# Performance work log

Hardware: AMD Instinct MI355X
Metric: run time of the kernel (lower is better)

## Reference

```python
import jax, jax.numpy as jnp
import numpy as np
from jax.scipy.linalg import expm

N_MODES, N_LAYERS, CUTOFF, BATCH = 6, 6, 3, 1024
M2 = N_MODES * (N_MODES - 1) // 2                  # beamsplitter thetas per interferometer
N_IF = N_MODES * (N_MODES - 1) + (N_MODES - 1)     # interferometer param count = 35

_np_a = np.diag(np.sqrt(np.arange(1, CUTOFF)), 1)  # truncated annihilation operator
A = jnp.asarray(_np_a, jnp.complex64)
AD = A.conj().T
NVEC = jnp.arange(CUTOFF, dtype=jnp.float32)       # number operator diagonal
X_OP = A + AD                                      # x quadrature (hbar=2, PennyLane/SF convention)
BS_GEN = jnp.kron(AD, A) - jnp.kron(A, AD)         # Beamsplitter(theta, 0) generator
SQ_GEN = A @ A - AD @ AD                           # Squeezing(r, 0) generator (times r/2)
D_GEN = AD - A                                     # Displacement(r, 0) generator

def disp_gate(r):
    return expm(r.astype(jnp.complex64) * D_GEN)

def sq_gate(r):
    return expm(0.5 * r.astype(jnp.complex64) * SQ_GEN)

def bs_gate(theta):
    return expm(theta.astype(jnp.complex64) * BS_GEN)

def apply_1(psi, U, m):
    # psi: (B, D, ..., D); apply DxD gate U on mode m
    psi = jnp.moveaxis(psi, 1 + m, -1)
    psi = psi @ U.T
    return jnp.moveaxis(psi, -1, 1 + m)

def apply_1_batched(psi, U, m):
    # U: (B, D, D) per-sample gate (data-encoding displacement)
    psi = jnp.moveaxis(psi, 1 + m, -1)
    psi = jnp.einsum('b...j,bij->b...i', psi, U)
    return jnp.moveaxis(psi, -1, 1 + m)

def apply_2(psi, U, m):
    psi = jnp.moveaxis(psi, (1 + m, 2 + m), (-2, -1))
    sh = psi.shape
    psi = (psi.reshape(sh[:-2] + (CUTOFF * CUTOFF,)) @ U.T).reshape(sh)
    return jnp.moveaxis(psi, (-2, -1), (1 + m, 2 + m))

def apply_diag(psi, d, m):
    shape = [1] * psi.ndim
    shape[1 + m] = CUTOFF
    return psi * d.reshape(shape)

def interferometer(psi, params):
    theta = params[:M2]
    rphi = params[-N_MODES:]  # faithful to source: overlaps last (unused) phi param
    n = 0
    for l in range(N_MODES):
        for k in range(N_MODES - 1):
            if (l + k) % 2 != 1:
                psi = apply_2(psi, bs_gate(theta[n]), k)
                n += 1
    for i in range(max(1, N_MODES - 1)):
        psi = apply_diag(psi, jnp.exp(1j * rphi[i] * NVEC), i)
    return psi

def cv_forward(x, theta_1, theta_2, squeezing_r, displacement_r, kerr_params):
    B = x.shape[0]
    psi = jnp.zeros((B,) + (CUTOFF,) * N_MODES, jnp.complex64)
    psi = psi.at[(slice(None),) + (0,) * N_MODES].set(1.0)  # |0...0> vacuum
    for m in range(N_MODES):  # data-encoding displacements, per-sample gates
        psi = apply_1_batched(psi, jax.vmap(disp_gate)(x[:, m]), m)
    for L in range(N_LAYERS):
        psi = interferometer(psi, theta_1[L])
        for m in range(N_MODES):
            psi = apply_1(psi, sq_gate(squeezing_r[L, m] * 0.5), m)
        psi = interferometer(psi, theta_2[L])
        for m in range(N_MODES):
            psi = apply_1(psi, disp_gate(displacement_r[L, m]), m)
            psi = apply_diag(psi, jnp.exp(1j * (kerr_params[L, m] * 0.001) * NVEC * NVEC), m)
    sum_axes = tuple(range(1, psi.ndim))
    outs = [jnp.sum(jnp.conj(psi) * apply_1(psi, X_OP, m), axis=sum_axes).real
            for m in range(N_MODES)]
    return jnp.stack(outs, axis=1)  # (B, N_MODES)

def setup_inputs() -> dict:
    key = jax.random.key(0)
    ks = jax.random.split(key, 6)
    passive_sd = 0.01 * np.pi
    return {
        'x': jax.random.normal(ks[0], (BATCH, N_MODES), jnp.float32),
        'theta_1': jax.random.normal(ks[1], (N_LAYERS, N_IF), jnp.float32) * passive_sd,
        'theta_2': jax.random.normal(ks[2], (N_LAYERS, N_IF), jnp.float32) * np.float32(0.2 * np.pi),
        'squeezing_r': jax.random.normal(ks[3], (N_LAYERS, N_MODES), jnp.float32) * 1e-3,
        'displacement_r': jax.random.normal(ks[4], (N_LAYERS, N_MODES), jnp.float32) * 1e-3,
        'kerr_params': jax.random.normal(ks[5], (N_LAYERS, N_MODES), jnp.float32) * 1e-3,
    }

def reference(x, theta_1, theta_2, squeezing_r, displacement_r, kerr_params):
    return cv_forward(x, theta_1, theta_2, squeezing_r, displacement_r, kerr_params)
```

## Files before the change

kernel.cpp:

```cpp
#include <hip/hip_runtime.h>

#define SQRT2f 1.41421356237309515f
#define SQRT3f 1.73205080756887729f

__device__ __forceinline__ float2 cmul(float2 a, float2 b) {
  return make_float2(a.x*b.x - a.y*b.y, a.x*b.y + a.y*b.x);
}
__device__ __forceinline__ float2 cadd(float2 a, float2 b) {
  return make_float2(a.x + b.x, a.y + b.y);
}

__device__ __forceinline__ void bs_q(float2 q[9], float2 cs) {
  const float c = cs.x, s = cs.y;
  const float c2 = c*c - s*s, s2 = 2.f*c*s;
  const float cc = c*c, ss = s*s, rcs = SQRT2f*c*s;
  float2 a1=q[1], a3=q[3], a2=q[2], a4=q[4], a6=q[6], a5=q[5], a7=q[7];
  q[1] = make_float2(c*a1.x - s*a3.x, c*a1.y - s*a3.y);
  q[3] = make_float2(s*a1.x + c*a3.x, s*a1.y + c*a3.y);
  q[2] = make_float2(cc*a2.x - rcs*a4.x + ss*a6.x, cc*a2.y - rcs*a4.y + ss*a6.y);
  q[4] = make_float2(rcs*a2.x + c2*a4.x - rcs*a6.x, rcs*a2.y + c2*a4.y - rcs*a6.y);
  q[6] = make_float2(ss*a2.x + rcs*a4.x + cc*a6.x, ss*a2.y + rcs*a4.y + cc*a6.y);
  q[5] = make_float2(c2*a5.x - s2*a7.x, c2*a5.y - s2*a7.y);
  q[7] = make_float2(s2*a5.x + c2*a7.x, s2*a5.y + c2*a7.y);
}

template<int SP>
__device__ __forceinline__ void bs_nonet(float2* __restrict__ psi, int base,
                                         float2 cs) {
  const float c = cs.x, s = cs.y;
  const float c2 = c*c - s*s, s2 = 2.f*c*s;
  const float cc = c*c, ss = s*s, rcs = SQRT2f*c*s;
  float2 a1 = psi[base+SP],   a3 = psi[base+3*SP];
  float2 a2 = psi[base+2*SP], a4 = psi[base+4*SP], a6 = psi[base+6*SP];
  float2 a5 = psi[base+5*SP], a7 = psi[base+7*SP];
  psi[base+SP]   = make_float2(c*a1.x - s*a3.x, c*a1.y - s*a3.y);
  psi[base+3*SP] = make_float2(s*a1.x + c*a3.x, s*a1.y + c*a3.y);
  psi[base+2*SP] = make_float2(cc*a2.x - rcs*a4.x + ss*a6.x,
                               cc*a2.y - rcs*a4.y + ss*a6.y);
  psi[base+4*SP] = make_float2(rcs*a2.x + c2*a4.x - rcs*a6.x,
                               rcs*a2.y + c2*a4.y - rcs*a6.y);
  psi[base+6*SP] = make_float2(ss*a2.x + rcs*a4.x + cc*a6.x,
                               ss*a2.y + rcs*a4.y + cc*a6.y);
  psi[base+5*SP] = make_float2(c2*a5.x - s2*a7.x, c2*a5.y - s2*a7.y);
  psi[base+7*SP] = make_float2(s2*a5.x + c2*a7.x, s2*a5.y + c2*a7.y);
}

template<int SP>
__device__ __forceinline__ void dpbs_nonet(float2* __restrict__ psi, int base,
                                           const float2* __restrict__ G,
                                           float2 cs) {
  const float2* A = G; const float2* B = G + 9;
  float2 v[3][3];
#pragma unroll
  for (int j = 0; j < 3; ++j)
#pragma unroll
    for (int jb = 0; jb < 3; ++jb) v[j][jb] = psi[base + j*3*SP + jb*SP];
  float2 t[3][3];
#pragma unroll
  for (int j = 0; j < 3; ++j)
#pragma unroll
    for (int ib = 0; ib < 3; ++ib)
      t[j][ib] = cadd(cadd(cmul(B[ib*3+0],v[j][0]), cmul(B[ib*3+1],v[j][1])),
                      cmul(B[ib*3+2],v[j][2]));
  float2 q[9];
#pragma unroll
  for (int i = 0; i < 3; ++i)
#pragma unroll
    for (int ib = 0; ib < 3; ++ib)
      q[i*3+ib] = cadd(cadd(cmul(A[i*3+0],t[0][ib]), cmul(A[i*3+1],t[1][ib])),
                       cmul(A[i*3+2],t[2][ib]));
  bs_q(q, cs);
#pragma unroll
  for (int i = 0; i < 3; ++i)
#pragma unroll
    for (int ib = 0; ib < 3; ++ib) psi[base + i*3*SP + ib*SP] = q[i*3+ib];
}

template<int SP>
__device__ __forceinline__ void sqbs_nonet(float2* __restrict__ psi, int base,
                                           const float2* __restrict__ G,
                                           float2 cs) {
  float2 A00=G[0],A02=G[1],A11=G[2],A20=G[3],A22=G[4];
  float2 B00=G[5],B02=G[6],B11=G[7],B20=G[8],B22=G[9];
  float2 v[3][3];
#pragma unroll
  for (int j = 0; j < 3; ++j)
#pragma unroll
    for (int jb = 0; jb < 3; ++jb) v[j][jb] = psi[base + j*3*SP + jb*SP];
  float2 t[3][3];
#pragma unroll
  for (int j = 0; j < 3; ++j) {
    t[j][0] = cadd(cmul(B00,v[j][0]), cmul(B02,v[j][2]));
    t[j][1] = cmul(B11,v[j][1]);
    t[j][2] = cadd(cmul(B20,v[j][0]), cmul(B22,v[j][2]));
  }
  float2 q[9];
#pragma unroll
  for (int ib = 0; ib < 3; ++ib) {
    q[ib]   = cadd(cmul(A00,t[0][ib]), cmul(A02,t[2][ib]));
    q[3+ib] = cmul(A11,t[1][ib]);
    q[6+ib] = cadd(cmul(A20,t[0][ib]), cmul(A22,t[2][ib]));
  }
  bs_q(q, cs);
#pragma unroll
  for (int i = 0; i < 3; ++i)
#pragma unroll
    for (int ib = 0; ib < 3; ++ib) psi[base + i*3*SP + ib*SP] = q[i*3+ib];
}

#define BASE4(g, s0,s1,s2,s3) ({ int _d=(g); int _b=(_d%3)*(s0); _d/=3; \
  _b += (_d%3)*(s1); _d/=3; _b += (_d%3)*(s2); _d/=3; _b += (_d%3)*(s3); _b; })
#define BASE5(g, s0,s1,s2,s3,s4) ({ int _d=(g); int _b=(_d%3)*(s0); _d/=3; \
  _b += (_d%3)*(s1); _d/=3; _b += (_d%3)*(s2); _d/=3; _b += (_d%3)*(s3); _d/=3; \
  _b += (_d%3)*(s4); _b; })

__device__ __forceinline__ float2 dpk_entry(const float* __restrict__ dr,
                                            const float* __restrict__ th2,
                                            const float* __restrict__ kp,
                                            int L, int mode, int i, int j) {
  float sn, cn; sincosf(SQRT3f*dr[L*6+mode], &sn, &cn);
  float sw = sn*(1.f/SQRT3f), cw = (1.f-cn)*(1.f/3.f);
  float U;
  if      (i==0) U = (j==0) ? (1.f-cw)     : (j==1) ? (-sw)         : (SQRT2f*cw);
  else if (i==1) U = (j==0) ? (sw)         : (j==1) ? (1.f-3.f*cw)  : (-SQRT2f*sw);
  else           U = (j==0) ? (SQRT2f*cw)  : (j==1) ? (SQRT2f*sw)   : (1.f-2.f*cw);
  float2 ph = make_float2(1.f, 0.f);
  if (mode < 5) { float ps, pc; sincosf(th2[L*35+29+mode], &ps, &pc);
                  ph = make_float2(pc, ps); }
  float2 phj = (j==0) ? make_float2(1.f,0.f) : (j==1) ? ph : cmul(ph, ph);
  float ks, kc; sincosf(0.001f*kp[L*6+mode], &ks, &kc);
  float2 k1 = make_float2(kc, ks);
  float2 ki = (i==0) ? make_float2(1.f,0.f)
            : (i==1) ? k1 : cmul(cmul(k1,k1), cmul(k1,k1));
  float2 t = cmul(phj, ki);
  return make_float2(U*t.x, U*t.y);
}

__global__ __launch_bounds__(128)
void cvnn_kernel(const float* __restrict__ x,
                 const float* __restrict__ th1,
                 const float* __restrict__ th2,
                 const float* __restrict__ sr,
                 const float* __restrict__ dr,
                 const float* __restrict__ kp,
                 float* __restrict__ out) {
  __shared__ float2 psi[729];
  __shared__ float2 gtab[690];
  __shared__ float red[12];

  const int tid = threadIdx.x;
  const int bidx = blockIdx.x;

  for (int f = tid; f < 690; f += 128) {
    float sn, cn; float2 v;
    if (f < 180) {
      int Lp = f/15, pos = f%15;
      int L = Lp/2, pass = Lp%2;
      float th = (pass ? th2 : th1)[L*35 + pos];
      sincosf(th, &sn, &cn); v = make_float2(cn, sn);
    } else if (f < 360) {
      int i = f - 180; int Lc = i/10, e = i%10;
      int L = Lc/3, c3 = Lc%3;
      int mode = 2*c3 + (e >= 5); int ee = e%5;
      float Sq, Cq; sincosf(0.25f*SQRT2f*sr[L*6+mode], &Sq, &Cq);
      float2 ph = make_float2(1.f, 0.f);
      if (mode < 5) { float ps, pc; sincosf(th1[L*35+29+mode], &ps, &pc);
                      ph = make_float2(pc, ps); }
      float2 ph2 = cmul(ph, ph);
      if      (ee == 0) v = make_float2(Cq, 0.f);
      else if (ee == 1) v = make_float2(Sq*ph2.x, Sq*ph2.y);
      else if (ee == 2) v = ph;
      else if (ee == 3) v = make_float2(-Sq, 0.f);
      else              v = make_float2(Cq*ph2.x, Cq*ph2.y);
    } else if (f < 630) {
      int i = f - 360; int Ld = i/18, e = i%18;
      int Ls = Ld/3, c3 = Ld%3;
      int mode = 2*c3 + (e >= 9); int ee = e%9;
      v = dpk_entry(dr, th2, kp, Ls, mode, ee/3, ee%3);
    } else if (f < 684) {
      int i = f - 630; int m = i/9, e = i%9;
      int ii = e/3, jj = e%3;
      float2 D0i = dpk_entry(dr, th2, kp, 5, m, 0, ii);
      float2 D1i = dpk_entry(dr, th2, kp, 5, m, 1, ii);
      float2 D2i = dpk_entry(dr, th2, kp, 5, m, 2, ii);
      float2 D0j = dpk_entry(dr, th2, kp, 5, m, 0, jj);
      float2 D1j = dpk_entry(dr, th2, kp, 5, m, 1, jj);
      float2 D2j = dpk_entry(dr, th2, kp, 5, m, 2, jj);
      float2 c0 = make_float2(D0i.x, -D0i.y);
      float2 c1 = make_float2(D1i.x, -D1i.y);
      float2 c2 = make_float2(D2i.x, -D2i.y);
      float2 acc = cmul(c0, D1j);
      float2 tmp = make_float2(D0j.x + SQRT2f*D2j.x, D0j.y + SQRT2f*D2j.y);
      acc = cadd(acc, cmul(c1, tmp));
      acc = cadd(acc, cmul(c2, make_float2(SQRT2f*D1j.x, SQRT2f*D1j.y)));
      v = acc;
    } else {
      int mode = f - 684;
      sincosf(SQRT3f*x[bidx*6 + mode], &sn, &cn);
      v = make_float2(sn*(1.f/SQRT3f), (1.f-cn)*(1.f/3.f));
    }
    gtab[f] = v;
  }
  __syncthreads();

  for (int idx = tid; idx < 729; idx += 128) {
    float pr = 1.f; int d = idx;
#pragma unroll
    for (int mm = 5; mm >= 0; --mm) {
      int n = d % 3; d /= 3;
      float2 dc = gtab[684 + mm];
      pr *= (n==0) ? (1.f-dc.y) : (n==1) ? dc.x : SQRT2f*dc.y;
    }
    psi[idx] = make_float2(pr, 0.f);
  }

  const bool act = (tid < 81);
  const int g = (tid < 81) ? tid : 0;
  const int b0 = g;
  const int b1 = BASE4(g, 1, 3, 9, 243);
  const int b2 = BASE4(g, 1, 3, 81, 243);
  const int b3 = BASE4(g, 1, 27, 81, 243);
  const int b4 = BASE4(g, 9, 27, 81, 243);
  __syncthreads();

  float2 csN = gtab[0];
  __syncthreads();

#define BSP(SP, BB, NEXT)  { if (act) bs_nonet<SP>(psi, BB, csN); \
    csN = gtab[NEXT]; __syncthreads(); }
#define DPBS(SP, BB, GI, NEXT) { if (act) dpbs_nonet<SP>(psi, BB, &gtab[GI], csN); \
    csN = gtab[NEXT]; __syncthreads(); }
#define SQBS(SP, BB, GI, NEXT) { if (act) sqbs_nonet<SP>(psi, BB, &gtab[GI], csN); \
    csN = gtab[NEXT]; __syncthreads(); }

#pragma unroll
  for (int L = 0; L < 6; ++L) {
    const int i1 = (L*2)*15, i2 = (L*2+1)*15;
    if (L == 0) {
      BSP(81, b0, i1+1); BSP(9, b2, i1+2); BSP(1, b4, i1+3);
    } else {
      const int gd = 360 + (L-1)*3*18;
      DPBS(81, b0, gd+0,  i1+1); DPBS(9, b2, gd+18, i1+2); DPBS(1, b4, gd+36, i1+3);
    }
    BSP(27, b1, i1+4);  BSP(3, b3, i1+5);
    BSP(81, b0, i1+6);  BSP(9, b2, i1+7);  BSP(1, b4, i1+8);
    BSP(27, b1, i1+9);  BSP(3, b3, i1+10);
    BSP(81, b0, i1+11); BSP(9, b2, i1+12); BSP(1, b4, i1+13);
    BSP(27, b1, i1+14); BSP(3, b3, i2+0);
    {
      const int gs = 180 + L*3*10;
      SQBS(81, b0, gs+0, i2+1); SQBS(9, b2, gs+10, i2+2); SQBS(1, b4, gs+20, i2+3);
    }
    BSP(27, b1, i2+4);  BSP(3, b3, i2+5);
    BSP(81, b0, i2+6);  BSP(9, b2, i2+7);  BSP(1, b4, i2+8);
    BSP(27, b1, i2+9);  BSP(3, b3, i2+10);
    BSP(81, b0, i2+11); BSP(9, b2, i2+12); BSP(1, b4, i2+13);
    BSP(27, b1, i2+14); BSP(3, b3, (L < 5) ? (L+1)*30 : 0);
  }

  float xs[6] = {0.f, 0.f, 0.f, 0.f, 0.f, 0.f};
  for (int it = 0; it < 2; ++it) {
    int t = tid + (it << 7);
    if (t < 243) {
#define XACC(m, SS, BB) { int b_ = (BB); \
      float2 a_ = psi[b_]; float2 e_ = psi[b_+(SS)]; float2 f_ = psi[b_+2*(SS)]; \
      const float2* M_ = &gtab[630 + (m)*9]; \
      float d0 = M_[0].x, d1 = M_[4].x, d2 = M_[8].x; \
      float2 M01 = M_[1], M02 = M_[2], M12 = M_[5]; \
      xs[m] += d0*(a_.x*a_.x + a_.y*a_.y) + d1*(e_.x*e_.x + e_.y*e_.y) \
             + d2*(f_.x*f_.x + f_.y*f_.y) \
        + 2.f*(M01.x*(a_.x*e_.x + a_.y*e_.y) - M01.y*(a_.x*e_.y - a_.y*e_.x)) \
        + 2.f*(M02.x*(a_.x*f_.x + a_.y*f_.y) - M02.y*(a_.x*f_.y - a_.y*f_.x)) \
        + 2.f*(M12.x*(e_.x*f_.x + e_.y*f_.y) - M12.y*(e_.x*f_.y - e_.y*f_.x)); }
      XACC(0, 243, BASE5(t, 1, 3, 9, 27, 81));
      XACC(1, 81,  BASE5(t, 1, 3, 9, 27, 243));
      XACC(2, 27,  BASE5(t, 1, 3, 9, 81, 243));
      XACC(3, 9,   BASE5(t, 1, 3, 27, 81, 243));
      XACC(4, 3,   BASE5(t, 1, 9, 27, 81, 243));
      XACC(5, 1,   BASE5(t, 3, 9, 27, 81, 243));
    }
  }
  const int lane = tid & 63, wid = tid >> 6;
#pragma unroll
  for (int m = 0; m < 6; ++m) {
    float v = xs[m];
    for (int off = 32; off > 0; off >>= 1) v += __shfl_down(v, off);
    if (lane == 0) red[wid*6 + m] = v;
  }
  __syncthreads();
  if (tid < 6) out[bidx*6 + tid] = red[tid] + red[6 + tid];
}

extern "C" void kernel_launch(void* const* d_in, const int* in_sizes, int n_in,
                              void* d_out, int out_size, void* d_ws, size_t ws_size,
                              hipStream_t stream) {
  const float* x  = (const float*)d_in[0];
  const float* t1 = (const float*)d_in[1];
  const float* t2 = (const float*)d_in[2];
  const float* sr = (const float*)d_in[3];
  const float* dr = (const float*)d_in[4];
  const float* kp = (const float*)d_in[5];
  const int B = in_sizes[0] / 6;
  cvnn_kernel<<<B, 128, 0, stream>>>(x, t1, t2, sr, dr, kp, (float*)d_out);
}
```

Before: 92.86 us.

## Process two batch samples per block to amortize gate table setup and barriers

Each block now simulates two batch samples, with separate shared-memory state vectors, instead of one. The gate table built from the shared parameters is computed once per pair, and each barrier-separated gate step updates both states using the same coefficients. This halves the grid size and the per-sample cost of table construction and synchronisation. The trade-off is doubled per-thread register and shared-memory use, which may lower occupancy, and only half as many blocks to fill the device.

```diff
diff --git a/kernel.cpp b/kernel.cpp
--- a/kernel.cpp
+++ b/kernel.cpp
@@ -10,10 +10,9 @@
   return make_float2(a.x + b.x, a.y + b.y);
 }
 
-__device__ __forceinline__ void bs_q(float2 q[9], float2 cs) {
-  const float c = cs.x, s = cs.y;
-  const float c2 = c*c - s*s, s2 = 2.f*c*s;
-  const float cc = c*c, ss = s*s, rcs = SQRT2f*c*s;
+__device__ __forceinline__ void bs_q(float2 q[9], float c, float s,
+                                     float c2, float s2, float cc, float ss,
+                                     float rcs) {
   float2 a1=q[1], a3=q[3], a2=q[2], a4=q[4], a6=q[6], a5=q[5], a7=q[7];
   q[1] = make_float2(c*a1.x - s*a3.x, c*a1.y - s*a3.y);
   q[3] = make_float2(s*a1.x + c*a3.x, s*a1.y + c*a3.y);
@@ -25,87 +24,155 @@
 }
 
 template<int SP>
-__device__ __forceinline__ void bs_nonet(float2* __restrict__ psi, int base,
-                                         float2 cs) {
+__device__ __forceinline__ void bs_nonet2(float2* __restrict__ pA,
+                                          float2* __restrict__ pB,
+                                          int base, float2 cs) {
   const float c = cs.x, s = cs.y;
   const float c2 = c*c - s*s, s2 = 2.f*c*s;
   const float cc = c*c, ss = s*s, rcs = SQRT2f*c*s;
-  float2 a1 = psi[base+SP],   a3 = psi[base+3*SP];
-  float2 a2 = psi[base+2*SP], a4 = psi[base+4*SP], a6 = psi[base+6*SP];
-  float2 a5 = psi[base+5*SP], a7 = psi[base+7*SP];
-  psi[base+SP]   = make_float2(c*a1.x - s*a3.x, c*a1.y - s*a3.y);
-  psi[base+3*SP] = make_float2(s*a1.x + c*a3.x, s*a1.y + c*a3.y);
-  psi[base+2*SP] = make_float2(cc*a2.x - rcs*a4.x + ss*a6.x,
-                               cc*a2.y - rcs*a4.y + ss*a6.y);
-  psi[base+4*SP] = make_float2(rcs*a2.x + c2*a4.x - rcs*a6.x,
-                               rcs*a2.y + c2*a4.y - rcs*a6.y);
-  psi[base+6*SP] = make_float2(ss*a2.x + rcs*a4.x + cc*a6.x,
-                               ss*a2.y + rcs*a4.y + cc*a6.y);
-  psi[base+5*SP] = make_float2(c2*a5.x - s2*a7.x, c2*a5.y - s2*a7.y);
-  psi[base+7*SP] = make_float2(s2*a5.x + c2*a7.x, s2*a5.y + c2*a7.y);
+  float2 A1 = pA[base+SP],   A3 = pA[base+3*SP];
+  float2 A2 = pA[base+2*SP], A4 = pA[base+4*SP], A6 = pA[base+6*SP];
+  float2 A5 = pA[base+5*SP], A7 = pA[base+7*SP];
+  float2 B1 = pB[base+SP],   B3 = pB[base+3*SP];
+  float2 B2 = pB[base+2*SP], B4 = pB[base+4*SP], B6 = pB[base+6*SP];
+  float2 B5 = pB[base+5*SP], B7 = pB[base+7*SP];
+  pA[base+SP]   = make_float2(c*A1.x - s*A3.x, c*A1.y - s*A3.y);
+  pA[base+3*SP] = make_float2(s*A1.x + c*A3.x, s*A1.y + c*A3.y);
+  pA[base+2*SP] = make_float2(cc*A2.x - rcs*A4.x + ss*A6.x,
+                              cc*A2.y - rcs*A4.y + ss*A6.y);
+  pA[base+4*SP] = make_float2(rcs*A2.x + c2*A4.x - rcs*A6.x,
+                              rcs*A2.y + c2*A4.y - rcs*A6.y);
+  pA[base+6*SP] = make_float2(ss*A2.x + rcs*A4.x + cc*A6.x,
+                              ss*A2.y + rcs*A4.y + cc*A6.y);
+  pA[base+5*SP] = make_float2(c2*A5.x - s2*A7.x, c2*A5.y - s2*A7.y);
+  pA[base+7*SP] = make_float2(s2*A5.x + c2*A7.x, s2*A5.y + c2*A7.y);
+  pB[base+SP]   = make_float2(c*B1.x - s*B3.x, c*B1.y - s*B3.y);
+  pB[base+3*SP] = make_float2(s*B1.x + c*B3.x, s*B1.y + c*B3.y);
+  pB[base+2*SP] = make_float2(cc*B2.x - rcs*B4.x + ss*B6.x,
+                              cc*B2.y - rcs*B4.y + ss*B6.y);
+  pB[base+4*SP] = make_float2(rcs*B2.x + c2*B4.x - rcs*B6.x,
+                              rcs*B2.y + c2*B4.y - rcs*B6.y);
+  pB[base+6*SP] = make_float2(ss*B2.x + rcs*B4.x + cc*B6.x,
+                              ss*B2.y + rcs*B4.y + cc*B6.y);
+  pB[base+5*SP] = make_float2(c2*B5.x - s2*B7.x, c2*B5.y - s2*B7.y);
+  pB[base+7*SP] = make_float2(s2*B5.x + c2*B7.x, s2*B5.y + c2*B7.y);
 }
 
 template<int SP>
-__device__ __forceinline__ void dpbs_nonet(float2* __restrict__ psi, int base,
-                                           const float2* __restrict__ G,
-                                           float2 cs) {
+__device__ __forceinline__ void dpbs_nonet2(float2* __restrict__ pA,
+                                            float2* __restrict__ pB,
+                                            int base,
+                                            const float2* __restrict__ G,
+                                            float2 cs) {
+  const float c = cs.x, s = cs.y;
+  const float c2 = c*c - s*s, s2 = 2.f*c*s;
+  const float cc = c*c, ss = s*s, rcs = SQRT2f*c*s;
   const float2* A = G; const float2* B = G + 9;
-  float2 v[3][3];
+  float2 vA[3][3], vB[3][3];
 #pragma unroll
   for (int j = 0; j < 3; ++j)
 #pragma unroll
-    for (int jb = 0; jb < 3; ++jb) v[j][jb] = psi[base + j*3*SP + jb*SP];
-  float2 t[3][3];
-#pragma unroll
-  for (int j = 0; j < 3; ++j)
-#pragma unroll
-    for (int ib = 0; ib < 3; ++ib)
-      t[j][ib] = cadd(cadd(cmul(B[ib*3+0],v[j][0]), cmul(B[ib*3+1],v[j][1])),
-                      cmul(B[ib*3+2],v[j][2]));
-  float2 q[9];
-#pragma unroll
-  for (int i = 0; i < 3; ++i)
-#pragma unroll
-    for (int ib = 0; ib < 3; ++ib)
-      q[i*3+ib] = cadd(cadd(cmul(A[i*3+0],t[0][ib]), cmul(A[i*3+1],t[1][ib])),
-                       cmul(A[i*3+2],t[2][ib]));
-  bs_q(q, cs);
-#pragma unroll
-  for (int i = 0; i < 3; ++i)
-#pragma unroll
-    for (int ib = 0; ib < 3; ++ib) psi[base + i*3*SP + ib*SP] = q[i*3+ib];
+    for (int jb = 0; jb < 3; ++jb) {
+      vA[j][jb] = pA[base + j*3*SP + jb*SP];
+      vB[j][jb] = pB[base + j*3*SP + jb*SP];
+    }
+  float2 qA[9], qB[9];
+  {
+    float2 t[3][3];
+#pragma unroll
+    for (int j = 0; j < 3; ++j)
+#pragma unroll
+      for (int ib = 0; ib < 3; ++ib)
+        t[j][ib] = cadd(cadd(cmul(B[ib*3+0],vA[j][0]), cmul(B[ib*3+1],vA[j][1])),
+                        cmul(B[ib*3+2],vA[j][2]));
+#pragma unroll
+    for (int i = 0; i < 3; ++i)
+#pragma unroll
+      for (int ib = 0; ib < 3; ++ib)
+        qA[i*3+ib] = cadd(cadd(cmul(A[i*3+0],t[0][ib]), cmul(A[i*3+1],t[1][ib])),
+                          cmul(A[i*3+2],t[2][ib]));
+  }
+  {
+    float2 t[3][3];
+#pragma unroll
+    for (int j = 0; j < 3; ++j)
+#pragma unroll
+      for (int ib = 0; ib < 3; ++ib)
+        t[j][ib] = cadd(cadd(cmul(B[ib*3+0],vB[j][0]), cmul(B[ib*3+1],vB[j][1])),
+                        cmul(B[ib*3+2],vB[j][2]));
+#pragma unroll
+    for (int i = 0; i < 3; ++i)
+#pragma unroll
+      for (int ib = 0; ib < 3; ++ib)
+        qB[i*3+ib] = cadd(cadd(cmul(A[i*3+0],t[0][ib]), cmul(A[i*3+1],t[1][ib])),
+                          cmul(A[i*3+2],t[2][ib]));
+  }
+  bs_q(qA, c, s, c2, s2, cc, ss, rcs);
+  bs_q(qB, c, s, c2, s2, cc, ss, rcs);
+#pragma unroll
+  for (int i = 0; i < 9; ++i) {
+    pA[base + (i/3)*3*SP + (i%3)*SP] = qA[i];
+    pB[base + (i/3)*3*SP + (i%3)*SP] = qB[i];
+  }
 }
 
 template<int SP>
-__device__ __forceinline__ void sqbs_nonet(float2* __restrict__ psi, int base,
-                                           const float2* __restrict__ G,
-                                           float2 cs) {
+__device__ __forceinline__ void sqbs_nonet2(float2* __restrict__ pA,
+                                            float2* __restrict__ pB,
+                                            int base,
+                                            const float2* __restrict__ G,
+                                            float2 cs) {
+  const float c = cs.x, s = cs.y;
+  const float c2 = c*c - s*s, s2 = 2.f*c*s;
+  const float cc = c*c, ss = s*s, rcs = SQRT2f*c*s;
   float2 A00=G[0],A02=G[1],A11=G[2],A20=G[3],A22=G[4];
   float2 B00=G[5],B02=G[6],B11=G[7],B20=G[8],B22=G[9];
-  float2 v[3][3];
+  float2 vA[3][3], vB[3][3];
 #pragma unroll
   for (int j = 0; j < 3; ++j)
 #pragma unroll
-    for (int jb = 0; jb < 3; ++jb) v[j][jb] = psi[base + j*3*SP + jb*SP];
-  float2 t[3][3];
-#pragma unroll
-  for (int j = 0; j < 3; ++j) {
-    t[j][0] = cadd(cmul(B00,v[j][0]), cmul(B02,v[j][2]));
-    t[j][1] = cmul(B11,v[j][1]);
-    t[j][2] = cadd(cmul(B20,v[j][0]), cmul(B22,v[j][2]));
-  }
-  float2 q[9];
-#pragma unroll
-  for (int ib = 0; ib < 3; ++ib) {
-    q[ib]   = cadd(cmul(A00,t[0][ib]), cmul(A02,t[2][ib]));
-    q[3+ib] = cmul(A11,t[1][ib]);
-    q[6+ib] = cadd(cmul(A20,t[0][ib]), cmul(A22,t[2][ib]));
-  }
-  bs_q(q, cs);
-#pragma unroll
-  for (int i = 0; i < 3; ++i)
-#pragma unroll
-    for (int ib = 0; ib < 3; ++ib) psi[base + i*3*SP + ib*SP] = q[i*3+ib];
+    for (int jb = 0; jb < 3; ++jb) {
+      vA[j][jb] = pA[base + j*3*SP + jb*SP];
+      vB[j][jb] = pB[base + j*3*SP + jb*SP];
+    }
+  float2 qA[9], qB[9];
+  {
+    float2 t[3][3];
+#pragma unroll
+    for (int j = 0; j < 3; ++j) {
+      t[j][0] = cadd(cmul(B00,vA[j][0]), cmul(B02,vA[j][2]));
+      t[j][1] = cmul(B11,vA[j][1]);
+      t[j][2] = cadd(cmul(B20,vA[j][0]), cmul(B22,vA[j][2]));
+    }
+#pragma unroll
+    for (int ib = 0; ib < 3; ++ib) {
+      qA[ib]   = cadd(cmul(A00,t[0][ib]), cmul(A02,t[2][ib]));
+      qA[3+ib] = cmul(A11,t[1][ib]);
+      qA[6+ib] = cadd(cmul(A20,t[0][ib]), cmul(A22,t[2][ib]));
+    }
+  }
+  {
+    float2 t[3][3];
+#pragma unroll
+    for (int j = 0; j < 3; ++j) {
+      t[j][0] = cadd(cmul(B00,vB[j][0]), cmul(B02,vB[j][2]));
+      t[j][1] = cmul(B11,vB[j][1]);
+      t[j][2] = cadd(cmul(B20,vB[j][0]), cmul(B22,vB[j][2]));
+    }
+#pragma unroll
+    for (int ib = 0; ib < 3; ++ib) {
+      qB[ib]   = cadd(cmul(A00,t[0][ib]), cmul(A02,t[2][ib]));
+      qB[3+ib] = cmul(A11,t[1][ib]);
+      qB[6+ib] = cadd(cmul(A20,t[0][ib]), cmul(A22,t[2][ib]));
+    }
+  }
+  bs_q(qA, c, s, c2, s2, cc, ss, rcs);
+  bs_q(qB, c, s, c2, s2, cc, ss, rcs);
+#pragma unroll
+  for (int i = 0; i < 9; ++i) {
+    pA[base + (i/3)*3*SP + (i%3)*SP] = qA[i];
+    pB[base + (i/3)*3*SP + (i%3)*SP] = qB[i];
+  }
 }
 
 #define BASE4(g, s0,s1,s2,s3) ({ int _d=(g); int _b=(_d%3)*(s0); _d/=3; \
@@ -143,15 +210,16 @@
                  const float* __restrict__ sr,
                  const float* __restrict__ dr,
                  const float* __restrict__ kp,
-                 float* __restrict__ out) {
-  __shared__ float2 psi[729];
-  __shared__ float2 gtab[690];
-  __shared__ float red[12];
+                 float* __restrict__ out, int Btot) {
+  __shared__ float2 psiA[729];
+  __shared__ float2 psiB[729];
+  __shared__ float2 gtab[696];
+  __shared__ float red[24];
 
   const int tid = threadIdx.x;
   const int bidx = blockIdx.x;
 
-  for (int f = tid; f < 690; f += 128) {
+  for (int f = tid; f < 696; f += 128) {
     float sn, cn; float2 v;
     if (f < 180) {
       int Lp = f/15, pos = f%15;
@@ -195,8 +263,9 @@
       acc = cadd(acc, cmul(c2, make_float2(SQRT2f*D1j.x, SQRT2f*D1j.y)));
       v = acc;
     } else {
-      int mode = f - 684;
-      sincosf(SQRT3f*x[bidx*6 + mode], &sn, &cn);
+      int i = f - 684; int st = i/6, mode = i%6;
+      int b = bidx*2 + st; if (b >= Btot) b = Btot - 1;
+      sincosf(SQRT3f*x[b*6 + mode], &sn, &cn);
       v = make_float2(sn*(1.f/SQRT3f), (1.f-cn)*(1.f/3.f));
     }
     gtab[f] = v;
@@ -204,14 +273,17 @@
   __syncthreads();
 
   for (int idx = tid; idx < 729; idx += 128) {
-    float pr = 1.f; int d = idx;
+    float prA = 1.f, prB = 1.f; int d = idx;
 #pragma unroll
     for (int mm = 5; mm >= 0; --mm) {
       int n = d % 3; d /= 3;
-      float2 dc = gtab[684 + mm];
-      pr *= (n==0) ? (1.f-dc.y) : (n==1) ? dc.x : SQRT2f*dc.y;
-    }
-    psi[idx] = make_float2(pr, 0.f);
+      float2 dA = gtab[684 + mm];
+      float2 dB = gtab[690 + mm];
+      prA *= (n==0) ? (1.f-dA.y) : (n==1) ? dA.x : SQRT2f*dA.y;
+      prB *= (n==0) ? (1.f-dB.y) : (n==1) ? dB.x : SQRT2f*dB.y;
+    }
+    psiA[idx] = make_float2(prA, 0.f);
+    psiB[idx] = make_float2(prB, 0.f);
   }
 
   const bool act = (tid < 81);
@@ -226,11 +298,11 @@
   float2 csN = gtab[0];
   __syncthreads();
 
-#define BSP(SP, BB, NEXT)  { if (act) bs_nonet<SP>(psi, BB, csN); \
+#define BSP(SP, BB, NEXT)  { if (act) bs_nonet2<SP>(psiA, psiB, BB, csN); \
     csN = gtab[NEXT]; __syncthreads(); }
-#define DPBS(SP, BB, GI, NEXT) { if (act) dpbs_nonet<SP>(psi, BB, &gtab[GI], csN); \
+#define DPBS(SP, BB, GI, NEXT) { if (act) dpbs_nonet2<SP>(psiA, psiB, BB, &gtab[GI], csN); \
     csN = gtab[NEXT]; __syncthreads(); }
-#define SQBS(SP, BB, GI, NEXT) { if (act) sqbs_nonet<SP>(psi, BB, &gtab[GI], csN); \
+#define SQBS(SP, BB, GI, NEXT) { if (act) sqbs_nonet2<SP>(psiA, psiB, BB, &gtab[GI], csN); \
     csN = gtab[NEXT]; __syncthreads(); }
 
 #pragma unroll
@@ -258,37 +330,51 @@
     BSP(27, b1, i2+14); BSP(3, b3, (L < 5) ? (L+1)*30 : 0);
   }
 
-  float xs[6] = {0.f, 0.f, 0.f, 0.f, 0.f, 0.f};
+  float xsA[6] = {0.f,0.f,0.f,0.f,0.f,0.f};
+  float xsB[6] = {0.f,0.f,0.f,0.f,0.f,0.f};
   for (int it = 0; it < 2; ++it) {
     int t = tid + (it << 7);
     if (t < 243) {
-#define XACC(m, SS, BB) { int b_ = (BB); \
-      float2 a_ = psi[b_]; float2 e_ = psi[b_+(SS)]; float2 f_ = psi[b_+2*(SS)]; \
+#define XACC2(m, SS, BB) { int b_ = (BB); \
       const float2* M_ = &gtab[630 + (m)*9]; \
       float d0 = M_[0].x, d1 = M_[4].x, d2 = M_[8].x; \
       float2 M01 = M_[1], M02 = M_[2], M12 = M_[5]; \
-      xs[m] += d0*(a_.x*a_.x + a_.y*a_.y) + d1*(e_.x*e_.x + e_.y*e_.y) \
-             + d2*(f_.x*f_.x + f_.y*f_.y) \
-        + 2.f*(M01.x*(a_.x*e_.x + a_.y*e_.y) - M01.y*(a_.x*e_.y - a_.y*e_.x)) \
-        + 2.f*(M02.x*(a_.x*f_.x + a_.y*f_.y) - M02.y*(a_.x*f_.y - a_.y*f_.x)) \
-        + 2.f*(M12.x*(e_.x*f_.x + e_.y*f_.y) - M12.y*(e_.x*f_.y - e_.y*f_.x)); }
-      XACC(0, 243, BASE5(t, 1, 3, 9, 27, 81));
-      XACC(1, 81,  BASE5(t, 1, 3, 9, 27, 243));
-      XACC(2, 27,  BASE5(t, 1, 3, 9, 81, 243));
-      XACC(3, 9,   BASE5(t, 1, 3, 27, 81, 243));
-      XACC(4, 3,   BASE5(t, 1, 9, 27, 81, 243));
-      XACC(5, 1,   BASE5(t, 3, 9, 27, 81, 243));
+      { float2 a_ = psiA[b_]; float2 e_ = psiA[b_+(SS)]; float2 f_ = psiA[b_+2*(SS)]; \
+        xsA[m] += d0*(a_.x*a_.x + a_.y*a_.y) + d1*(e_.x*e_.x + e_.y*e_.y) \
+               + d2*(f_.x*f_.x + f_.y*f_.y) \
+          + 2.f*(M01.x*(a_.x*e_.x + a_.y*e_.y) - M01.y*(a_.x*e_.y - a_.y*e_.x)) \
+          + 2.f*(M02.x*(a_.x*f_.x + a_.y*f_.y) - M02.y*(a_.x*f_.y - a_.y*f_.x)) \
+          + 2.f*(M12.x*(e_.x*f_.x + e_.y*f_.y) - M12.y*(e_.x*f_.y - e_.y*f_.x)); } \
+      { float2 a_ = psiB[b_]; float2 e_ = psiB[b_+(SS)]; float2 f_ = psiB[b_+2*(SS)]; \
+        xsB[m] += d0*(a_.x*a_.x + a_.y*a_.y) + d1*(e_.x*e_.x + e_.y*e_.y) \
+               + d2*(f_.x*f_.x + f_.y*f_.y) \
+          + 2.f*(M01.x*(a_.x*e_.x + a_.y*e_.y) - M01.y*(a_.x*e_.y - a_.y*e_.x)) \
+          + 2.f*(M02.x*(a_.x*f_.x + a_.y*f_.y) - M02.y*(a_.x*f_.y - a_.y*f_.x)) \
+          + 2.f*(M12.x*(e_.x*f_.x + e_.y*f_.y) - M12.y*(e_.x*f_.y - e_.y*f_.x)); } }
+      XACC2(0, 243, BASE5(t, 1, 3, 9, 27, 81));
+      XACC2(1, 81,  BASE5(t, 1, 3, 9, 27, 243));
+      XACC2(2, 27,  BASE5(t, 1, 3, 9, 81, 243));
+      XACC2(3, 9,   BASE5(t, 1, 3, 27, 81, 243));
+      XACC2(4, 3,   BASE5(t, 1, 9, 27, 81, 243));
+      XACC2(5, 1,   BASE5(t, 3, 9, 27, 81, 243));
     }
   }
   const int lane = tid & 63, wid = tid >> 6;
 #pragma unroll
   for (int m = 0; m < 6; ++m) {
-    float v = xs[m];
-    for (int off = 32; off > 0; off >>= 1) v += __shfl_down(v, off);
-    if (lane == 0) red[wid*6 + m] = v;
+    float vA = xsA[m], vB = xsB[m];
+    for (int off = 32; off > 0; off >>= 1) {
+      vA += __shfl_down(vA, off); vB += __shfl_down(vB, off);
+    }
+    if (lane == 0) { red[wid*6 + m] = vA; red[12 + wid*6 + m] = vB; }
   }
   __syncthreads();
-  if (tid < 6) out[bidx*6 + tid] = red[tid] + red[6 + tid];
+  if (tid < 12) {
+    int st = tid/6, m = tid%6;
+    float v = red[st*12 + m] + red[st*12 + 6 + m];
+    int b = bidx*2 + st;
+    if (b < Btot) out[b*6 + m] = v;
+  }
 }
 
 extern "C" void kernel_launch(void* const* d_in, const int* in_sizes, int n_in,
@@ -301,5 +387,6 @@
   const float* dr = (const float*)d_in[4];
   const float* kp = (const float*)d_in[5];
   const int B = in_sizes[0] / 6;
-  cvnn_kernel<<<B, 128, 0, stream>>>(x, t1, t2, sr, dr, kp, (float*)d_out);
-}
+  const int nb = (B + 1) / 2;
+  cvnn_kernel<<<nb, 128, 0, stream>>>(x, t1, t2, sr, dr, kp, (float*)d_out, B);
+}
```

Measured after the change: 128.8 us. 38.7% more time.

## Fuse beamsplitter stages into 27-element cube sweeps to cut barrier count

Applied to the files above, without the earlier changes.

Replaces the per-beamsplitter passes (one 81-thread pass and one barrier per gate) with grouped passes. Each of 27 threads loads a 27-element sub-cube over three modes and applies two or three consecutive gates in registers, including the folded displacement/squeezing matrices. The number of shared-memory round trips and __syncthreads per layer falls from 15 to 9. In exchange, only 27 threads are active in those phases, so parallelism drops and register pressure rises because each thread holds 27 complex values.

```diff
diff --git a/kernel.cpp b/kernel.cpp
--- a/kernel.cpp
+++ b/kernel.cpp
@@ -10,10 +10,9 @@
   return make_float2(a.x + b.x, a.y + b.y);
 }
 
-__device__ __forceinline__ void bs_q(float2 q[9], float2 cs) {
-  const float c = cs.x, s = cs.y;
-  const float c2 = c*c - s*s, s2 = 2.f*c*s;
-  const float cc = c*c, ss = s*s, rcs = SQRT2f*c*s;
+__device__ __forceinline__ void bs_q(float2* q, float c, float s,
+                                     float c2, float s2, float cc, float ss,
+                                     float rcs) {
   float2 a1=q[1], a3=q[3], a2=q[2], a4=q[4], a6=q[6], a5=q[5], a7=q[7];
   q[1] = make_float2(c*a1.x - s*a3.x, c*a1.y - s*a3.y);
   q[3] = make_float2(s*a1.x + c*a3.x, s*a1.y + c*a3.y);
@@ -46,70 +45,144 @@
 }
 
 template<int SP>
+__device__ __forceinline__ void sqbs_nonet(float2* __restrict__ psi, int base,
+                                           const float2* __restrict__ G,
+                                           float2 cs) {
+  const float c = cs.x, s = cs.y;
+  const float c2 = c*c - s*s, s2 = 2.f*c*s;
+  const float cc = c*c, ss = s*s, rcs = SQRT2f*c*s;
+  float2 A00=G[0],A02=G[1],A11=G[2],A20=G[3],A22=G[4];
+  float2 B00=G[5],B02=G[6],B11=G[7],B20=G[8],B22=G[9];
+  float2 v[3][3];
+#pragma unroll
+  for (int j = 0; j < 3; ++j)
+#pragma unroll
+    for (int jb = 0; jb < 3; ++jb) v[j][jb] = psi[base + j*3*SP + jb*SP];
+  float2 q[9];
+  {
+    float2 t[3][3];
+#pragma unroll
+    for (int j = 0; j < 3; ++j) {
+      t[j][0] = cadd(cmul(B00,v[j][0]), cmul(B02,v[j][2]));
+      t[j][1] = cmul(B11,v[j][1]);
+      t[j][2] = cadd(cmul(B20,v[j][0]), cmul(B22,v[j][2]));
+    }
+#pragma unroll
+    for (int ib = 0; ib < 3; ++ib) {
+      q[ib]   = cadd(cmul(A00,t[0][ib]), cmul(A02,t[2][ib]));
+      q[3+ib] = cmul(A11,t[1][ib]);
+      q[6+ib] = cadd(cmul(A20,t[0][ib]), cmul(A22,t[2][ib]));
+    }
+  }
+  bs_q(q, c, s, c2, s2, cc, ss, rcs);
+#pragma unroll
+  for (int i = 0; i < 9; ++i) psi[base + (i/3)*3*SP + (i%3)*SP] = q[i];
+}
+
+template<int SP>
 __device__ __forceinline__ void dpbs_nonet(float2* __restrict__ psi, int base,
                                            const float2* __restrict__ G,
                                            float2 cs) {
+  const float c = cs.x, s = cs.y;
+  const float c2 = c*c - s*s, s2 = 2.f*c*s;
+  const float cc = c*c, ss = s*s, rcs = SQRT2f*c*s;
   const float2* A = G; const float2* B = G + 9;
   float2 v[3][3];
 #pragma unroll
   for (int j = 0; j < 3; ++j)
 #pragma unroll
     for (int jb = 0; jb < 3; ++jb) v[j][jb] = psi[base + j*3*SP + jb*SP];
-  float2 t[3][3];
-#pragma unroll
-  for (int j = 0; j < 3; ++j)
-#pragma unroll
-    for (int ib = 0; ib < 3; ++ib)
-      t[j][ib] = cadd(cadd(cmul(B[ib*3+0],v[j][0]), cmul(B[ib*3+1],v[j][1])),
-                      cmul(B[ib*3+2],v[j][2]));
   float2 q[9];
-#pragma unroll
-  for (int i = 0; i < 3; ++i)
-#pragma unroll
-    for (int ib = 0; ib < 3; ++ib)
-      q[i*3+ib] = cadd(cadd(cmul(A[i*3+0],t[0][ib]), cmul(A[i*3+1],t[1][ib])),
-                       cmul(A[i*3+2],t[2][ib]));
-  bs_q(q, cs);
-#pragma unroll
-  for (int i = 0; i < 3; ++i)
-#pragma unroll
-    for (int ib = 0; ib < 3; ++ib) psi[base + i*3*SP + ib*SP] = q[i*3+ib];
-}
-
-template<int SP>
-__device__ __forceinline__ void sqbs_nonet(float2* __restrict__ psi, int base,
+  {
+    float2 t[3][3];
+#pragma unroll
+    for (int j = 0; j < 3; ++j)
+#pragma unroll
+      for (int ib = 0; ib < 3; ++ib)
+        t[j][ib] = cadd(cadd(cmul(B[ib*3+0],v[j][0]), cmul(B[ib*3+1],v[j][1])),
+                        cmul(B[ib*3+2],v[j][2]));
+#pragma unroll
+    for (int i = 0; i < 3; ++i)
+#pragma unroll
+      for (int ib = 0; ib < 3; ++ib)
+        q[i*3+ib] = cadd(cadd(cmul(A[i*3+0],t[0][ib]), cmul(A[i*3+1],t[1][ib])),
+                         cmul(A[i*3+2],t[2][ib]));
+  }
+  bs_q(q, c, s, c2, s2, cc, ss, rcs);
+#pragma unroll
+  for (int i = 0; i < 9; ++i) psi[base + (i/3)*3*SP + (i%3)*SP] = q[i];
+}
+
+template<int ST, int FOLD>
+__device__ __forceinline__ void cube_sweep(float2* __restrict__ psi, int base,
                                            const float2* __restrict__ G,
-                                           float2 cs) {
-  float2 A00=G[0],A02=G[1],A11=G[2],A20=G[3],A22=G[4];
-  float2 B00=G[5],B02=G[6],B11=G[7],B20=G[8],B22=G[9];
-  float2 v[3][3];
-#pragma unroll
-  for (int j = 0; j < 3; ++j)
-#pragma unroll
-    for (int jb = 0; jb < 3; ++jb) v[j][jb] = psi[base + j*3*SP + jb*SP];
-  float2 t[3][3];
-#pragma unroll
-  for (int j = 0; j < 3; ++j) {
-    t[j][0] = cadd(cmul(B00,v[j][0]), cmul(B02,v[j][2]));
-    t[j][1] = cmul(B11,v[j][1]);
-    t[j][2] = cadd(cmul(B20,v[j][0]), cmul(B22,v[j][2]));
-  }
-  float2 q[9];
-#pragma unroll
-  for (int ib = 0; ib < 3; ++ib) {
-    q[ib]   = cadd(cmul(A00,t[0][ib]), cmul(A02,t[2][ib]));
-    q[3+ib] = cmul(A11,t[1][ib]);
-    q[6+ib] = cadd(cmul(A20,t[0][ib]), cmul(A22,t[2][ib]));
-  }
-  bs_q(q, cs);
-#pragma unroll
-  for (int i = 0; i < 3; ++i)
-#pragma unroll
-    for (int ib = 0; ib < 3; ++ib) psi[base + i*3*SP + ib*SP] = q[i*3+ib];
-}
-
-#define BASE4(g, s0,s1,s2,s3) ({ int _d=(g); int _b=(_d%3)*(s0); _d/=3; \
-  _b += (_d%3)*(s1); _d/=3; _b += (_d%3)*(s2); _d/=3; _b += (_d%3)*(s3); _b; })
+                                           float2 csM, float2 csH) {
+  float2 v[27];
+#pragma unroll
+  for (int r = 0; r < 27; ++r) v[r] = psi[base + ST*r];
+  if (FOLD == 1) {
+    float2 A00=G[0],A02=G[1],A11=G[2],A20=G[3],A22=G[4];
+    float2 B00=G[5],B02=G[6],B11=G[7],B20=G[8],B22=G[9];
+#pragma unroll
+    for (int t = 0; t < 9; ++t) {
+      float2 u0=v[t*3], u2=v[t*3+2];
+      v[t*3]   = cadd(cmul(B00,u0), cmul(B02,u2));
+      v[t*3+1] = cmul(B11, v[t*3+1]);
+      v[t*3+2] = cadd(cmul(B20,u0), cmul(B22,u2));
+    }
+#pragma unroll
+    for (int h = 0; h < 3; ++h)
+#pragma unroll
+      for (int lo = 0; lo < 3; ++lo) {
+        int rb = h*9 + lo;
+        float2 u0=v[rb], u2=v[rb+6];
+        v[rb]   = cadd(cmul(A00,u0), cmul(A02,u2));
+        v[rb+3] = cmul(A11, v[rb+3]);
+        v[rb+6] = cadd(cmul(A20,u0), cmul(A22,u2));
+      }
+  }
+  if (FOLD == 2) {
+#pragma unroll
+    for (int t = 0; t < 9; ++t) {
+      float2 u0=v[t*3], u1=v[t*3+1], u2=v[t*3+2];
+      v[t*3]   = cadd(cadd(cmul(G[9+0],u0),cmul(G[9+1],u1)),cmul(G[9+2],u2));
+      v[t*3+1] = cadd(cadd(cmul(G[9+3],u0),cmul(G[9+4],u1)),cmul(G[9+5],u2));
+      v[t*3+2] = cadd(cadd(cmul(G[9+6],u0),cmul(G[9+7],u1)),cmul(G[9+8],u2));
+    }
+#pragma unroll
+    for (int h = 0; h < 3; ++h)
+#pragma unroll
+      for (int lo = 0; lo < 3; ++lo) {
+        int rb = h*9 + lo;
+        float2 u0=v[rb], u1=v[rb+3], u2=v[rb+6];
+        v[rb]   = cadd(cadd(cmul(G[0],u0),cmul(G[1],u1)),cmul(G[2],u2));
+        v[rb+3] = cadd(cadd(cmul(G[3],u0),cmul(G[4],u1)),cmul(G[5],u2));
+        v[rb+6] = cadd(cadd(cmul(G[6],u0),cmul(G[7],u1)),cmul(G[8],u2));
+      }
+  }
+  {
+    const float c=csM.x, s=csM.y;
+    const float c2=c*c-s*s, s2=2.f*c*s, cc=c*c, ss=s*s, rcs=SQRT2f*c*s;
+#pragma unroll
+    for (int h = 0; h < 3; ++h) bs_q(&v[h*9], c, s, c2, s2, cc, ss, rcs);
+  }
+  {
+    const float c=csH.x, s=csH.y;
+    const float c2=c*c-s*s, s2=2.f*c*s, cc=c*c, ss=s*s, rcs=SQRT2f*c*s;
+#pragma unroll
+    for (int lo = 0; lo < 3; ++lo) {
+      float2 q[9];
+#pragma unroll
+      for (int j = 0; j < 9; ++j) q[j] = v[(j/3)*9 + (j%3)*3 + lo];
+      bs_q(q, c, s, c2, s2, cc, ss, rcs);
+#pragma unroll
+      for (int j = 0; j < 9; ++j) v[(j/3)*9 + (j%3)*3 + lo] = q[j];
+    }
+  }
+#pragma unroll
+  for (int r = 0; r < 27; ++r) psi[base + ST*r] = v[r];
+}
+
 #define BASE5(g, s0,s1,s2,s3,s4) ({ int _d=(g); int _b=(_d%3)*(s0); _d/=3; \
   _b += (_d%3)*(s1); _d/=3; _b += (_d%3)*(s2); _d/=3; _b += (_d%3)*(s3); _d/=3; \
   _b += (_d%3)*(s4); _b; })
@@ -214,59 +287,69 @@
     psi[idx] = make_float2(pr, 0.f);
   }
 
-  const bool act = (tid < 81);
   const int g = (tid < 81) ? tid : 0;
   const int b0 = g;
-  const int b1 = BASE4(g, 1, 3, 9, 243);
-  const int b2 = BASE4(g, 1, 3, 81, 243);
-  const int b3 = BASE4(g, 1, 27, 81, 243);
-  const int b4 = BASE4(g, 9, 27, 81, 243);
+  const int h = (tid < 27) ? tid : 0;
+  const int n0h = h/9, hm = (h%9)/3, hl = h%3;
+  const int base123 = n0h*243 + hm*3 + hl;
+  const int base345 = n0h*243 + hm*81 + hl*27;
   __syncthreads();
 
-  float2 csN = gtab[0];
-  __syncthreads();
-
-#define BSP(SP, BB, NEXT)  { if (act) bs_nonet<SP>(psi, BB, csN); \
-    csN = gtab[NEXT]; __syncthreads(); }
-#define DPBS(SP, BB, GI, NEXT) { if (act) dpbs_nonet<SP>(psi, BB, &gtab[GI], csN); \
-    csN = gtab[NEXT]; __syncthreads(); }
-#define SQBS(SP, BB, GI, NEXT) { if (act) sqbs_nonet<SP>(psi, BB, &gtab[GI], csN); \
-    csN = gtab[NEXT]; __syncthreads(); }
+#define W81_BS(GI)      { if (tid < 81) bs_nonet<81>(psi, b0, gtab[GI]); \
+    __syncthreads(); }
+#define W81_SQBS(GS,GI) { if (tid < 81) sqbs_nonet<81>(psi, b0, &gtab[GS], gtab[GI]); \
+    __syncthreads(); }
+#define W81_DPBS(GD,GI) { if (tid < 81) dpbs_nonet<81>(psi, b0, &gtab[GD], gtab[GI]); \
+    __syncthreads(); }
+#define W27_123(F,GP,GI1,GI2) { if (tid < 27) \
+    cube_sweep<9,F>(psi, base123, GP, gtab[GI1], gtab[GI2]); __syncthreads(); }
+#define W27_345(F,GP,GI1,GI2) { if (tid < 27) \
+    cube_sweep<1,F>(psi, base345, GP, gtab[GI1], gtab[GI2]); __syncthreads(); }
 
 #pragma unroll
   for (int L = 0; L < 6; ++L) {
-    const int i1 = (L*2)*15, i2 = (L*2+1)*15;
-    if (L == 0) {
-      BSP(81, b0, i1+1); BSP(9, b2, i1+2); BSP(1, b4, i1+3);
-    } else {
-      const int gd = 360 + (L-1)*3*18;
-      DPBS(81, b0, gd+0,  i1+1); DPBS(9, b2, gd+18, i1+2); DPBS(1, b4, gd+36, i1+3);
-    }
-    BSP(27, b1, i1+4);  BSP(3, b3, i1+5);
-    BSP(81, b0, i1+6);  BSP(9, b2, i1+7);  BSP(1, b4, i1+8);
-    BSP(27, b1, i1+9);  BSP(3, b3, i1+10);
-    BSP(81, b0, i1+11); BSP(9, b2, i1+12); BSP(1, b4, i1+13);
-    BSP(27, b1, i1+14); BSP(3, b3, i2+0);
     {
-      const int gs = 180 + L*3*10;
-      SQBS(81, b0, gs+0, i2+1); SQBS(9, b2, gs+10, i2+2); SQBS(1, b4, gs+20, i2+3);
-    }
-    BSP(27, b1, i2+4);  BSP(3, b3, i2+5);
-    BSP(81, b0, i2+6);  BSP(9, b2, i2+7);  BSP(1, b4, i2+8);
-    BSP(27, b1, i2+9);  BSP(3, b3, i2+10);
-    BSP(81, b0, i2+11); BSP(9, b2, i2+12); BSP(1, b4, i2+13);
-    BSP(27, b1, i2+14); BSP(3, b3, (L < 5) ? (L+1)*30 : 0);
-  }
-
-  float xs[6] = {0.f, 0.f, 0.f, 0.f, 0.f, 0.f};
+      const int PB = (L*2)*15;
+      if (L == 0) {
+        W81_BS(PB+0);
+        W27_123(0, (const float2*)nullptr, PB+1, PB+3);
+        W27_345(0, (const float2*)nullptr, PB+2, PB+4);
+      } else {
+        const int gd = 360 + (L-1)*54;
+        W81_DPBS(gd+0, PB+0);
+        W27_123(2, &gtab[gd+18], PB+1, PB+3);
+        W27_345(2, &gtab[gd+36], PB+2, PB+4);
+      }
+      W81_BS(PB+5);
+      W27_123(0, (const float2*)nullptr, PB+6, PB+8);
+      W27_345(0, (const float2*)nullptr, PB+7, PB+9);
+      W81_BS(PB+10);
+      W27_123(0, (const float2*)nullptr, PB+11, PB+13);
+      W27_345(0, (const float2*)nullptr, PB+12, PB+14);
+    }
+    {
+      const int PB = (L*2+1)*15, gs = 180 + L*30;
+      W81_SQBS(gs+0, PB+0);
+      W27_123(1, &gtab[gs+10], PB+1, PB+3);
+      W27_345(1, &gtab[gs+20], PB+2, PB+4);
+      W81_BS(PB+5);
+      W27_123(0, (const float2*)nullptr, PB+6, PB+8);
+      W27_345(0, (const float2*)nullptr, PB+7, PB+9);
+      W81_BS(PB+10);
+      W27_123(0, (const float2*)nullptr, PB+11, PB+13);
+      W27_345(0, (const float2*)nullptr, PB+12, PB+14);
+    }
+  }
+
+  float xs[6] = {0.f,0.f,0.f,0.f,0.f,0.f};
   for (int it = 0; it < 2; ++it) {
     int t = tid + (it << 7);
     if (t < 243) {
 #define XACC(m, SS, BB) { int b_ = (BB); \
-      float2 a_ = psi[b_]; float2 e_ = psi[b_+(SS)]; float2 f_ = psi[b_+2*(SS)]; \
       const float2* M_ = &gtab[630 + (m)*9]; \
       float d0 = M_[0].x, d1 = M_[4].x, d2 = M_[8].x; \
       float2 M01 = M_[1], M02 = M_[2], M12 = M_[5]; \
+      float2 a_ = psi[b_]; float2 e_ = psi[b_+(SS)]; float2 f_ = psi[b_+2*(SS)]; \
       xs[m] += d0*(a_.x*a_.x + a_.y*a_.y) + d1*(e_.x*e_.x + e_.y*e_.y) \
              + d2*(f_.x*f_.x + f_.y*f_.y) \
         + 2.f*(M01.x*(a_.x*e_.x + a_.y*e_.y) - M01.y*(a_.x*e_.y - a_.y*e_.x)) \
```

After: 109.1 us. 17.5% more time.
